# Kernel optimization log

Hardware: AMD Instinct MI355X
Metric: run time of the kernel (lower is better)

## Reference

```python
import jax, jax.numpy as jnp
import numpy as np

N_WORDS, MAX_CHARS = 32768, 16
WORD_DIM, CHAR_DIM, HIDDEN = 256, 64, 256
VOCAB = 256


def setup_inputs() -> dict:
    key = jax.random.key(0)
    ks = jax.random.split(key, 10)
    char_indices = jax.random.randint(ks[0], (N_WORDS, MAX_CHARS), 0, VOCAB)
    char_lengths = jax.random.randint(ks[1], (N_WORDS,), 1, MAX_CHARS + 1)
    word_emb = jax.random.normal(ks[2], (N_WORDS, WORD_DIM), dtype=jnp.float32)
    s = 0.05
    E_char = jax.random.normal(ks[3], (VOCAB, CHAR_DIM), dtype=jnp.float32) * s
    W_ih = jax.random.normal(ks[4], (4 * HIDDEN, CHAR_DIM), dtype=jnp.float32) * s
    W_hh = jax.random.normal(ks[5], (4 * HIDDEN, HIDDEN), dtype=jnp.float32) * s
    b_ih = jax.random.normal(ks[6], (4 * HIDDEN,), dtype=jnp.float32) * s
    b_hh = jax.random.normal(ks[7], (4 * HIDDEN,), dtype=jnp.float32) * s
    W_lin = jax.random.normal(ks[8], (WORD_DIM, WORD_DIM + HIDDEN), dtype=jnp.float32) * s
    b_lin = jax.random.normal(ks[9], (WORD_DIM,), dtype=jnp.float32) * s
    return dict(char_indices=char_indices, char_lengths=char_lengths,
                word_emb=word_emb, E_char=E_char, W_ih=W_ih, W_hh=W_hh,
                b_ih=b_ih, b_hh=b_hh, W_lin=W_lin, b_lin=b_lin)


def _lstm_last_hidden(x, lengths, W_ih, W_hh, b_ih, b_hh):
    # x: [N, T, E]; returns final hidden h at position length-1 per row.
    N, T, _ = x.shape
    H = W_hh.shape[1]
    x_proj = jnp.einsum('nte,ge->ntg', x, W_ih) + (b_ih + b_hh)  # [N, T, 4H]
    x_proj = jnp.transpose(x_proj, (1, 0, 2))                    # time-major [T, N, 4H]

    def step(carry, inp):
        h, c = carry
        xg, t = inp
        gates = xg + h @ W_hh.T
        i, f, g, o = jnp.split(gates, 4, axis=-1)
        i, f, o = jax.nn.sigmoid(i), jax.nn.sigmoid(f), jax.nn.sigmoid(o)
        g = jnp.tanh(g)
        c_new = f * c + i * g
        h_new = o * jnp.tanh(c_new)
        mask = (t < lengths)[:, None]  # freeze state past each word's length
        h = jnp.where(mask, h_new, h)
        c = jnp.where(mask, c_new, c)
        return (h, c), None

    h0 = jnp.zeros((N, H), dtype=x.dtype)
    c0 = jnp.zeros((N, H), dtype=x.dtype)
    (h, _), _ = jax.lax.scan(step, (h0, c0), (x_proj, jnp.arange(T)))
    return h


def reference(char_indices, char_lengths, word_emb, E_char, W_ih, W_hh,
              b_ih, b_hh, W_lin, b_lin):
    char_embedded = E_char[char_indices]                        # [N, T, E]
    h = _lstm_last_hidden(char_embedded, char_lengths, W_ih, W_hh, b_ih, b_hh)
    combined = jnp.concatenate([word_emb, h], axis=-1)          # [N, WORD+H]
    return jax.nn.relu(combined @ W_lin.T + b_lin)              # [N, WORD]
```

## Files before the change

### kernel.cpp

```cpp
#include <hip/hip_runtime.h>


#define NW 32768

typedef __attribute__((ext_vector_type(8))) short short8;
typedef __attribute__((ext_vector_type(4))) float f32x4;
typedef __attribute__((ext_vector_type(4))) int i32x4;

#define MFMA16(a,b,c) __builtin_amdgcn_mfma_f32_16x16x32_bf16(a,b,c,0,0,0)
#define MFMAI8(a,b,c) __builtin_amdgcn_mfma_i32_16x16x32_i8(a,b,c,0,0,0)

#define O_ORDER 0
#define O_SLEN  131072
#define O_WPK   262144
#define O_USTP  524288
#define O_WLIN  528384
#define O_PX    790528
#define O_BH    1839104
#define O_BASE  1847296

__device__ inline unsigned short f2b(float f) {
  unsigned u = __builtin_bit_cast(unsigned, f);
  u = u + 0x7fffu + ((u >> 16) & 1u);
  return (unsigned short)(u >> 16);
}
__device__ inline float fsigm(float x) {
  float e = __builtin_amdgcn_exp2f(-1.44269504f * x);
  return __builtin_amdgcn_rcpf(1.0f + e);
}
__device__ inline float ftanh(float x) {
  float e = __builtin_amdgcn_exp2f(2.88539008f * x);
  return 1.0f - 2.0f * __builtin_amdgcn_rcpf(e + 1.0f);
}

__global__ void k_prep0(const float* __restrict__ whh, unsigned char* __restrict__ ws) {
  int i = blockIdx.x * 256 + threadIdx.x;
  const f32x4* r4 = (const f32x4*)(whh + i * 256);
  float mx = 0.f;
  #pragma unroll 8
  for (int k4 = 0; k4 < 64; ++k4) {
    f32x4 v = r4[k4];
    mx = fmaxf(mx, fmaxf(fmaxf(fabsf(v[0]), fabsf(v[1])),
                         fmaxf(fabsf(v[2]), fabsf(v[3]))));
  }
  ((float*)(ws + O_USTP))[i] = mx / (127.f * 127.f);
}

__global__ void k_prep1(const float* __restrict__ whh, const float* __restrict__ wlin,
                        unsigned char* __restrict__ ws) {
  int i = blockIdx.x * 256 + threadIdx.x;
  if (i < 262144) {
    int j = i & 7, lane = (i >> 3) & 63, t2 = i >> 9;
    int nt = t2 & 7, u2 = t2 >> 3;
    int kb = u2 & 7, w = u2 >> 3;
    int n = (nt >> 1) * 256 + w * 32 + (nt & 1) * 16 + (lane & 15);
    int k = kb * 32 + (lane >> 4) * 8 + j;
    float v = whh[n * 256 + k];
    float ustep = ((const float*)(ws + O_USTP))[n] * 127.f;
    float qf = (ustep > 0.f) ? v / ustep : 0.f;
    int q = (int)__builtin_rintf(qf);
    q = q < -127 ? -127 : (q > 127 ? 127 : q);
    ((signed char*)(ws + O_WPK))[i] = (signed char)q;
    return;
  }
  int i2 = i - 262144;
  {
    int j = i2 & 7, lane = (i2 >> 3) & 63, t3 = i2 >> 9;
    int kf = t3 & 15, nn = t3 >> 4;
    int n = (nn >> 2) * 64 + (nn & 3) * 16 + (lane & 15);
    int k = kf * 32 + (lane >> 4) * 8 + j;
    ((unsigned short*)(ws + O_WLIN))[i2] = f2b(wlin[n * 512 + k]);
  }
}

__global__ void k_prep2(const float* __restrict__ wih, const float* __restrict__ ech,
                        const float* __restrict__ bih, const float* __restrict__ bhh,
                        unsigned char* __restrict__ ws) {
  int id = blockIdx.x * 256 + threadIdx.x;
  int c = id >> 10, n = id & 1023;
  const f32x4* w4 = (const f32x4*)(wih + n * 64);
  const f32x4* e4 = (const f32x4*)(ech + c * 64);
  float acc = bih[n] + bhh[n];
  #pragma unroll
  for (int k4 = 0; k4 < 16; ++k4) {
    f32x4 a = w4[k4], e = e4[k4];
    acc += a[0] * e[0] + a[1] * e[1] + a[2] * e[2] + a[3] * e[3];
  }
  ((float*)(ws + O_PX))[((c << 8) + (n & 255)) * 4 + (n >> 8)] = acc;
}

__global__ void k_hist(const int* __restrict__ lens, unsigned char* __restrict__ ws) {
  __shared__ int h[16];
  int t = threadIdx.x, b = blockIdx.x;
  if (t < 16) h[t] = 0;
  __syncthreads();
  int wid = b * 256 + t;
  int l = lens[wid]; l = l < 1 ? 1 : (l > 16 ? 16 : l);
  atomicAdd(&h[l - 1], 1);
  __syncthreads();
  if (t < 16) ((int*)(ws + O_BH))[b * 16 + t] = h[t];
}

__global__ void k_scan(unsigned char* __restrict__ ws) {
  __shared__ int tot[16], g[16];
  int t = threadIdx.x;
  const int* bh = (const int*)(ws + O_BH);
  int* base = (int*)(ws + O_BASE);
  if (t < 16) {
    int s = 0;
    for (int b = 0; b < 128; ++b) s += bh[b * 16 + t];
    tot[t] = s;
  }
  __syncthreads();
  if (t == 0) { int a = 0; for (int i = 0; i < 16; ++i) { g[i] = a; a += tot[i]; } }
  __syncthreads();
  if (t < 16) {
    int run = g[t];
    for (int b = 0; b < 128; ++b) { base[b * 16 + t] = run; run += bh[b * 16 + t]; }
  }
}

__global__ void k_scatter(const int* __restrict__ lens, unsigned char* __restrict__ ws) {
  __shared__ int cnt[16];
  int t = threadIdx.x, b = blockIdx.x;
  if (t < 16) cnt[t] = 0;
  __syncthreads();
  int wid = b * 256 + t;
  int l = lens[wid]; l = l < 1 ? 1 : (l > 16 ? 16 : l);
  int rank = atomicAdd(&cnt[l - 1], 1);
  int p = ((const int*)(ws + O_BASE))[b * 16 + (l - 1)] + rank;
  ((int*)(ws + O_ORDER))[p] = wid;
  ((int*)(ws + O_SLEN))[p] = l;
}

__global__ __launch_bounds__(512, 2) void k_main(
    const int* __restrict__ cidx, const float* __restrict__ wemb,
    const float* __restrict__ blin, float* __restrict__ outp,
    const unsigned char* __restrict__ ws) {
  __shared__ signed char Xb[2][4][8][64][8];
  __shared__ int CW[64][16];

  const int tid = threadIdx.x, b = blockIdx.x;
  const int w = tid >> 6, lane = tid & 63;
  const int q = lane >> 4, l15 = lane & 15;

  const int* order = (const int*)(ws + O_ORDER);
  const int* slen  = (const int*)(ws + O_SLEN);
  const signed char* wpk = (const signed char*)(ws + O_WPK);
  const float* upt = (const float*)(ws + O_USTP);
  const unsigned short* wlin = (const unsigned short*)(ws + O_WLIN);
  const float* pxt = (const float*)(ws + O_PX);

  long wreg[8][8];
  #pragma unroll
  for (int kb = 0; kb < 8; ++kb)
    #pragma unroll
    for (int nt = 0; nt < 8; ++nt)
      wreg[kb][nt] = *(const long*)(wpk + (((w * 8 + kb) * 8 + nt) * 64 + lane) * 8);

  float uq[8];
  #pragma unroll
  for (int nt = 0; nt < 8; ++nt) {
    int n = (nt >> 1) * 256 + w * 32 + (nt & 1) * 16 + l15;
    uq[nt] = upt[n];
  }
  const int hd0 = w * 32 + l15;
  const int mh = w >> 2, nw = w & 3;
  float blv[4];
  #pragma unroll
  for (int nt = 0; nt < 4; ++nt) blv[nt] = blin[nw * 64 + nt * 16 + l15];

  for (int sl = 0; sl < 2; ++sl) {
    const int s = sl ? (511 - b) : b;
    const int base = 64 * s;
    __syncthreads();
    {
      long* p = (long*)&Xb[0][0][0][0][0];
      #pragma unroll
      for (int ii = 0; ii < 4; ++ii) p[tid + 512 * ii] = 0L;
    }
    if (tid < 256) {
      int m = tid >> 2, part = tid & 3;
      int wid = order[base + m];
      *(i32x4*)&CW[m][part * 4] = *(const i32x4*)(cidx + wid * 16 + part * 4);
    }
    int tmax[4]; unsigned lenpk[4];
    #pragma unroll
    for (int mt = 0; mt < 4; ++mt) {
      int pbm = base + 16 * mt;
      tmax[mt] = slen[pbm + 15];
      unsigned l0 = (unsigned)slen[pbm + q * 4 + 0];
      unsigned l1 = (unsigned)slen[pbm + q * 4 + 1];
      unsigned l2 = (unsigned)slen[pbm + q * 4 + 2];
      unsigned l3 = (unsigned)slen[pbm + q * 4 + 3];
      lenpk[mt] = l0 | (l1 << 8) | (l2 << 16) | (l3 << 24);
    }
    const int Tm = tmax[3];
    __syncthreads();

    float creg[4][2][4];
    unsigned hreg[4][2];
    #pragma unroll
    for (int mt = 0; mt < 4; ++mt)
      #pragma unroll
      for (int hs = 0; hs < 2; ++hs) {
        hreg[mt][hs] = 0u;
        #pragma unroll
        for (int r = 0; r < 4; ++r) creg[mt][hs][r] = 0.f;
      }

    for (int t = 0; t < Tm; ++t) {
      const int rd = t & 1, wb = rd ^ 1;
      #pragma unroll
      for (int mt = 0; mt < 4; ++mt) {
        if (mt != 3 && t >= tmax[mt]) continue;
        int cc[4];
        #pragma unroll
        for (int r = 0; r < 4; ++r) cc[r] = CW[mt * 16 + q * 4 + r][t] & 255;
        #pragma unroll
        for (int hs = 0; hs < 2; ++hs) {
          f32x4 pxv[4];
          #pragma unroll
          for (int r = 0; r < 4; ++r)
            pxv[r] = *(const f32x4*)&pxt[((cc[r] << 8) + hd0 + hs * 16) * 4];
          i32x4 a0 = (i32x4)0, a1 = (i32x4)0, a2 = (i32x4)0, a3 = (i32x4)0;
          #pragma unroll
          for (int kb = 0; kb < 8; ++kb) {
            long A = *(const long*)&Xb[rd][mt][kb][lane][0];
            a0 = MFMAI8(A, wreg[kb][0 + hs], a0);
            a1 = MFMAI8(A, wreg[kb][2 + hs], a1);
            a2 = MFMAI8(A, wreg[kb][4 + hs], a2);
            a3 = MFMAI8(A, wreg[kb][6 + hs], a3);
          }
          unsigned hp = 0;
          #pragma unroll
          for (int r = 0; r < 4; ++r) {
            float gi = (float)a0[r] * uq[0 + hs] + pxv[r][0];
            float gf = (float)a1[r] * uq[2 + hs] + pxv[r][1];
            float gg = (float)a2[r] * uq[4 + hs] + pxv[r][2];
            float go = (float)a3[r] * uq[6 + hs] + pxv[r][3];
            float si = fsigm(gi), sf = fsigm(gf);
            float sg = ftanh(gg), so = fsigm(go);
            float cold = creg[mt][hs][r];
            float cn = sf * cold + si * sg;
            float hn = so * ftanh(cn);
            int lene = (int)((lenpk[mt] >> (8 * r)) & 255u);
            bool live = t < lene;
            creg[mt][hs][r] = live ? cn : cold;
            int hq = (int)__builtin_rintf(127.f * hn);
            unsigned ob = (hreg[mt][hs] >> (8 * r)) & 255u;
            unsigned nb = live ? ((unsigned)hq & 255u) : ob;
            hp |= nb << (8 * r);
          }
          hreg[mt][hs] = hp;
        }
      }

      #pragma unroll
      for (int mt = 0; mt < 4; ++mt) {
        if (mt != 3 && t >= tmax[mt]) continue;
        #pragma unroll
        for (int hs = 0; hs < 2; ++hs) {
          int row16 = 16 * (hs * 2 + (l15 >> 3));
          #pragma unroll
          for (int r = 0; r < 4; ++r)
            Xb[wb][mt][w][(q * 4 + r) + row16][l15 & 7] =
                (signed char)((hreg[mt][hs] >> (8 * r)) & 255u);
        }
      }
      __syncthreads();
    }

    int widA[2];
    #pragma unroll
    for (int mi = 0; mi < 2; ++mi) widA[mi] = order[base + (2 * mh + mi) * 16 + l15];
    const int tb0 = (mh ? tmax[2] : tmax[0]) & 1;
    const int tb1 = (mh ? tmax[3] : tmax[1]) & 1;
    f32x4 fac[2][4];
    #pragma unroll
    for (int mi = 0; mi < 2; ++mi)
      #pragma unroll
      for (int nt = 0; nt < 4; ++nt) fac[mi][nt] = 0.0f;

    #pragma unroll
    for (int kf = 0; kf < 16; ++kf) {
      short8 Bn[4];
      #pragma unroll
      for (int nt = 0; nt < 4; ++nt)
        Bn[nt] = ((const short8*)wlin)[((nw * 4 + nt) * 16 + kf) * 64 + lane];
      short8 Am[2];
      #pragma unroll
      for (int mi = 0; mi < 2; ++mi) {
        if (kf < 8) {
          const f32x4* pa = (const f32x4*)(wemb + widA[mi] * 256 + kf * 32 + q * 8);
          f32x4 f0 = pa[0], f1 = pa[1];
          short8 A;
          A[0] = (short)f2b(f0[0]); A[1] = (short)f2b(f0[1]);
          A[2] = (short)f2b(f0[2]); A[3] = (short)f2b(f0[3]);
          A[4] = (short)f2b(f1[0]); A[5] = (short)f2b(f1[1]);
          A[6] = (short)f2b(f1[2]); A[7] = (short)f2b(f1[3]);
          Am[mi] = A;
        } else {
          int mtv = 2 * mh + mi;
          int tb = mi ? tb1 : tb0;
          long ch = *(const long*)&Xb[tb][mtv][kf - 8][lane][0];
          short8 A;
          #pragma unroll
          for (int j = 0; j < 8; ++j) {
            int v = (int)(signed char)((ch >> (8 * j)) & 255);
            A[j] = (short)f2b((float)v * (1.f / 127.f));
          }
          Am[mi] = A;
        }
      }
      #pragma unroll
      for (int mi = 0; mi < 2; ++mi)
        #pragma unroll
        for (int nt = 0; nt < 4; ++nt)
          fac[mi][nt] = MFMA16(Am[mi], Bn[nt], fac[mi][nt]);
    }
    #pragma unroll
    for (int mi = 0; mi < 2; ++mi) {
      #pragma unroll
      for (int r = 0; r < 4; ++r) {
        int wid = order[base + (2 * mh + mi) * 16 + q * 4 + r];
        float* po = outp + wid * 256 + nw * 64 + l15;
        #pragma unroll
        for (int nt = 0; nt < 4; ++nt) {
          float v = fac[mi][nt][r] + blv[nt];
          po[nt * 16] = v > 0.f ? v : 0.f;
        }
      }
    }
  }
}

extern "C" void kernel_launch(void* const* d_in, const int* in_sizes, int n_in,
                              void* d_out, int out_size, void* d_ws, size_t ws_size,
                              hipStream_t stream) {
  const int*   cidx = (const int*)d_in[0];
  const int*   clen = (const int*)d_in[1];
  const float* wemb = (const float*)d_in[2];
  const float* ech  = (const float*)d_in[3];
  const float* wih  = (const float*)d_in[4];
  const float* whh  = (const float*)d_in[5];
  const float* bih  = (const float*)d_in[6];
  const float* bhh  = (const float*)d_in[7];
  const float* wlin = (const float*)d_in[8];
  const float* blin = (const float*)d_in[9];
  float* outp = (float*)d_out;
  unsigned char* ws = (unsigned char*)d_ws;

  k_prep0<<<4, 256, 0, stream>>>(whh, ws);
  k_prep1<<<1536, 256, 0, stream>>>(whh, wlin, ws);
  k_prep2<<<1024, 256, 0, stream>>>(wih, ech, bih, bhh, ws);
  k_hist<<<128, 256, 0, stream>>>(clen, ws);
  k_scan<<<1, 64, 0, stream>>>(ws);
  k_scatter<<<128, 256, 0, stream>>>(clen, ws);
  k_main<<<256, 512, 0, stream>>>(cidx, wemb, blin, outp, ws);
}
```

Baseline: 410.1 us.

## Store precomputed input-gate table in bf16 and use nontemporal streaming loads/stores

The per-character input projection table (char x gate) is now stored as bf16 instead of fp32, which halves its size and the gather traffic inside the recurrent loop; the values are expanded back to fp32 on load. Streaming accesses (char indices, word embeddings, output writes) now use nontemporal hints so they do not evict the reused table and weights from cache. The launch-bounds occupancy hint is also restated through the waves_per_eu attribute. Storing the table in bf16 adds rounding error to the gate pre-activations.

Result: no change. 402.5 us (-1.9%).

```diff
diff --git a/kernel.cpp b/kernel.cpp
--- a/kernel.cpp
+++ b/kernel.cpp
@@ -6,6 +6,7 @@
 typedef __attribute__((ext_vector_type(8))) short short8;
 typedef __attribute__((ext_vector_type(4))) float f32x4;
 typedef __attribute__((ext_vector_type(4))) int i32x4;
+typedef __attribute__((ext_vector_type(4))) unsigned short u16x4;
 
 #define MFMA16(a,b,c) __builtin_amdgcn_mfma_f32_16x16x32_bf16(a,b,c,0,0,0)
 #define MFMAI8(a,b,c) __builtin_amdgcn_mfma_i32_16x16x32_i8(a,b,c,0,0,0)
@@ -16,13 +17,16 @@
 #define O_USTP  524288
 #define O_WLIN  528384
 #define O_PX    790528
-#define O_BH    1839104
-#define O_BASE  1847296
+#define O_BH    1314816
+#define O_BASE  1323008
 
 __device__ inline unsigned short f2b(float f) {
   unsigned u = __builtin_bit_cast(unsigned, f);
   u = u + 0x7fffu + ((u >> 16) & 1u);
   return (unsigned short)(u >> 16);
+}
+__device__ inline float b2f(unsigned short u) {
+  return __builtin_bit_cast(float, ((unsigned)u) << 16);
 }
 __device__ inline float fsigm(float x) {
   float e = __builtin_amdgcn_exp2f(-1.44269504f * x);
@@ -86,7 +90,7 @@
     f32x4 a = w4[k4], e = e4[k4];
     acc += a[0] * e[0] + a[1] * e[1] + a[2] * e[2] + a[3] * e[3];
   }
-  ((float*)(ws + O_PX))[((c << 8) + (n & 255)) * 4 + (n >> 8)] = acc;
+  ((unsigned short*)(ws + O_PX))[((c << 8) + (n & 255)) * 4 + (n >> 8)] = f2b(acc);
 }
 
 __global__ void k_hist(const int* __restrict__ lens, unsigned char* __restrict__ ws) {
@@ -133,7 +137,9 @@
   ((int*)(ws + O_SLEN))[p] = l;
 }
 
-__global__ __launch_bounds__(512, 2) void k_main(
+__global__ __launch_bounds__(512)
+__attribute__((amdgpu_waves_per_eu(2, 2)))
+void k_main(
     const int* __restrict__ cidx, const float* __restrict__ wemb,
     const float* __restrict__ blin, float* __restrict__ outp,
     const unsigned char* __restrict__ ws) {
@@ -149,7 +155,7 @@
   const signed char* wpk = (const signed char*)(ws + O_WPK);
   const float* upt = (const float*)(ws + O_USTP);
   const unsigned short* wlin = (const unsigned short*)(ws + O_WLIN);
-  const float* pxt = (const float*)(ws + O_PX);
+  const unsigned short* pxt = (const unsigned short*)(ws + O_PX);
 
   long wreg[8][8];
   #pragma unroll
@@ -182,7 +188,8 @@
     if (tid < 256) {
       int m = tid >> 2, part = tid & 3;
       int wid = order[base + m];
-      *(i32x4*)&CW[m][part * 4] = *(const i32x4*)(cidx + wid * 16 + part * 4);
+      *(i32x4*)&CW[m][part * 4] =
+          __builtin_nontemporal_load((const i32x4*)(cidx + wid * 16 + part * 4));
     }
     int tmax[4]; unsigned lenpk[4];
     #pragma unroll
@@ -219,10 +226,10 @@
         for (int r = 0; r < 4; ++r) cc[r] = CW[mt * 16 + q * 4 + r][t] & 255;
         #pragma unroll
         for (int hs = 0; hs < 2; ++hs) {
-          f32x4 pxv[4];
+          u16x4 pb[4];
           #pragma unroll
           for (int r = 0; r < 4; ++r)
-            pxv[r] = *(const f32x4*)&pxt[((cc[r] << 8) + hd0 + hs * 16) * 4];
+            pb[r] = *(const u16x4*)&pxt[((cc[r] << 8) + hd0 + hs * 16) * 4];
           i32x4 a0 = (i32x4)0, a1 = (i32x4)0, a2 = (i32x4)0, a3 = (i32x4)0;
           #pragma unroll
           for (int kb = 0; kb < 8; ++kb) {
@@ -235,10 +242,10 @@
           unsigned hp = 0;
           #pragma unroll
           for (int r = 0; r < 4; ++r) {
-            float gi = (float)a0[r] * uq[0 + hs] + pxv[r][0];
-            float gf = (float)a1[r] * uq[2 + hs] + pxv[r][1];
-            float gg = (float)a2[r] * uq[4 + hs] + pxv[r][2];
-            float go = (float)a3[r] * uq[6 + hs] + pxv[r][3];
+            float gi = (float)a0[r] * uq[0 + hs] + b2f(pb[r][0]);
+            float gf = (float)a1[r] * uq[2 + hs] + b2f(pb[r][1]);
+            float gg = (float)a2[r] * uq[4 + hs] + b2f(pb[r][2]);
+            float go = (float)a3[r] * uq[6 + hs] + b2f(pb[r][3]);
             float si = fsigm(gi), sf = fsigm(gf);
             float sg = ftanh(gg), so = fsigm(go);
             float cold = creg[mt][hs][r];
@@ -293,7 +300,8 @@
       for (int mi = 0; mi < 2; ++mi) {
         if (kf < 8) {
           const f32x4* pa = (const f32x4*)(wemb + widA[mi] * 256 + kf * 32 + q * 8);
-          f32x4 f0 = pa[0], f1 = pa[1];
+          f32x4 f0 = __builtin_nontemporal_load(pa);
+          f32x4 f1 = __builtin_nontemporal_load(pa + 1);
           short8 A;
           A[0] = (short)f2b(f0[0]); A[1] = (short)f2b(f0[1]);
           A[2] = (short)f2b(f0[2]); A[3] = (short)f2b(f0[3]);
@@ -328,7 +336,7 @@
         #pragma unroll
         for (int nt = 0; nt < 4; ++nt) {
           float v = fac[mi][nt][r] + blv[nt];
-          po[nt * 16] = v > 0.f ? v : 0.f;
+          __builtin_nontemporal_store(v > 0.f ? v : 0.f, po + nt * 16);
         }
       }
     }
```
